# Performance work log

Measured on AMD Instinct MI355X. Metric: run time of the kernel, lower is better.

## Reference

```python
import jax, jax.numpy as jnp
import numpy as np

N_NODES = 50000
N_EDGES = 800000
IN_F = 128
HID = 32
HEADS = 8
N_CLASSES = 40
OUT_HEADS = 1
NEG_SLOPE = 0.2


def _glorot(key, shape):
    fan_in, fan_out = shape[0], int(np.prod(shape[1:]))
    s = jnp.sqrt(6.0 / (fan_in + fan_out))
    return jax.random.uniform(key, shape, jnp.float32, -s, s)


def setup_inputs() -> dict:
    key = jax.random.key(0)
    ks = jax.random.split(key, 12)
    x = jax.random.normal(ks[0], (N_NODES, IN_F), jnp.float32)
    src = jax.random.randint(ks[1], (N_EDGES,), 0, N_NODES, jnp.int32)
    dst = jax.random.randint(ks[2], (N_EDGES,), 0, N_NODES, jnp.int32)
    # layer 1: IN_F -> HEADS*HID
    W1 = _glorot(ks[3], (IN_F, HEADS * HID))
    al1 = _glorot(ks[4], (HEADS, HID))
    ar1 = _glorot(ks[5], (HEADS, HID))
    # layer 2: HEADS*HID -> HEADS*HID
    W2 = _glorot(ks[6], (HEADS * HID, HEADS * HID))
    al2 = _glorot(ks[7], (HEADS, HID))
    ar2 = _glorot(ks[8], (HEADS, HID))
    # output layer: HEADS*HID -> OUT_HEADS*N_CLASSES (mean over heads)
    Wo = _glorot(ks[9], (HEADS * HID, OUT_HEADS * N_CLASSES))
    alo = _glorot(ks[10], (OUT_HEADS, N_CLASSES))
    aro = _glorot(ks[11], (OUT_HEADS, N_CLASSES))
    return dict(x=x, src=src, dst=dst, W1=W1, al1=al1, ar1=ar1,
                W2=W2, al2=al2, ar2=ar2, Wo=Wo, alo=alo, aro=aro)


def gat_conv(x, src, dst, W, al, ar, concat):
    """Standard GAT layer: per-head projection, edge attention, segment softmax, scatter-sum."""
    N = x.shape[0]
    H, F = al.shape
    h = (x @ W).reshape(N, H, F)                         # [N,H,F]
    el = jnp.einsum('nhf,hf->nh', h, al)                 # [N,H]
    er = jnp.einsum('nhf,hf->nh', h, ar)                 # [N,H]
    e = jax.nn.leaky_relu(el[src] + er[dst], NEG_SLOPE)  # [E,H]
    m = jax.ops.segment_max(e, dst, num_segments=N)      # [N,H] per-dst max
    ex = jnp.exp(e - m[dst])                             # [E,H]
    s = jax.ops.segment_sum(ex, dst, num_segments=N)     # [N,H]
    alpha = ex / (s[dst] + 1e-16)                        # [E,H] softmax over in-edges
    out = jax.ops.segment_sum(h[src] * alpha[:, :, None], dst, num_segments=N)  # [N,H,F]
    return out.reshape(N, H * F) if concat else out.mean(axis=1)


def reference(x, src, dst, W1, al1, ar1, W2, al2, ar2, Wo, alo, aro):
    h = jax.nn.elu(gat_conv(x, src, dst, W1, al1, ar1, concat=True))
    h = jax.nn.elu(gat_conv(h, src, dst, W2, al2, ar2, concat=True))
    out = gat_conv(h, src, dst, Wo, alo, aro, concat=False)  # [N, N_CLASSES]
    return jax.nn.log_softmax(out, axis=1)
```

## Files before the change

### kernel.cpp

```cpp
#include <hip/hip_runtime.h>
#include <hip/hip_bf16.h>

#define N_NODES 50000
#define N_EDGES 800000

typedef __bf16 bf16x8 __attribute__((ext_vector_type(8)));
typedef float f32x4 __attribute__((ext_vector_type(4)));
typedef float f32x2 __attribute__((ext_vector_type(2)));

__device__ __forceinline__ float loadF(const void* p, size_t i, bool isbf) {
    return isbf ? __bfloat162float(((const __hip_bfloat16*)p)[i]) : ((const float*)p)[i];
}
__device__ __forceinline__ float bfbits2f(unsigned short u) {
    return __uint_as_float(((unsigned)u) << 16);
}
__device__ __forceinline__ unsigned short f2bfbits(float f) {
    __hip_bfloat16 h = __float2bfloat16(f);
    return *(unsigned short*)&h;
}
__device__ __forceinline__ void acc8_fp8(float ex, uint2 r, float* acc) {
    f32x2 p0 = __builtin_amdgcn_cvt_pk_f32_fp8(r.x, false);
    f32x2 p1 = __builtin_amdgcn_cvt_pk_f32_fp8(r.x, true);
    f32x2 p2 = __builtin_amdgcn_cvt_pk_f32_fp8(r.y, false);
    f32x2 p3 = __builtin_amdgcn_cvt_pk_f32_fp8(r.y, true);
    acc[0] += ex * p0.x; acc[1] += ex * p0.y;
    acc[2] += ex * p1.x; acc[3] += ex * p1.y;
    acc[4] += ex * p2.x; acc[5] += ex * p2.y;
    acc[6] += ex * p3.x; acc[7] += ex * p3.y;
}

__global__ void cvt_hist_k(const void* __restrict__ x, const void* __restrict__ W1,
                           const void* __restrict__ W2, const void* __restrict__ Wo,
                           unsigned short* __restrict__ Xb, unsigned short* __restrict__ W1f,
                           unsigned short* __restrict__ W2f, unsigned short* __restrict__ Wof,
                           int* __restrict__ flag, const int* __restrict__ dst,
                           int* __restrict__ cursor, unsigned short* __restrict__ erank) {
    __shared__ int s_flag;
    int t = threadIdx.x;
    if (t < 64) {
        const unsigned short* xw = (const unsigned short*)x;
        int cnt = 0;
        for (int i = t; i < 512; i += 64) {
            unsigned e = (xw[2 * i] >> 7) & 0xFFu;
            if (e >= 117u && e <= 134u) cnt++;
        }
        for (int off = 32; off; off >>= 1) cnt += __shfl_down(cnt, off, 64);
        if (t == 0) s_flag = (cnt >= 256) ? 1 : 0;
    }
    __syncthreads();
    bool bf = (s_flag != 0);
    int i = blockIdx.x * blockDim.x + t;
    if (i == 0) *flag = s_flag ? 1 : 0;
    if (i < 800000) {
        if (!bf) {
            const float* f = (const float*)x + (size_t)i * 8;
            unsigned short r[8];
            for (int j = 0; j < 8; ++j) r[j] = f2bfbits(f[j]);
            *(uint4*)(Xb + (size_t)i * 8) = *(uint4*)r;
        }
        return;
    }
    int u = i - 800000;
    if (u >= 14336) {
        int e = u - 14336;
        if (e < N_EDGES) {
            int r = atomicAdd(&cursor[dst[e]], 1);
            erank[e] = (unsigned short)r;
        }
        return;
    }
    const void* W; unsigned short* dstp; int Nf, Npad, s, rem;
    if (u < 4096)        { W = W1; dstp = W1f; Nf = 256; Npad = 256; s = u / 1024; rem = u % 1024; }
    else if (u < 12288)  { u -= 4096;  W = W2; dstp = W2f; Nf = 256; Npad = 256; s = u / 1024; rem = u % 1024; }
    else                 { u -= 12288; W = Wo; dstp = Wof; Nf = 40;  Npad = 64;  s = u / 256;  rem = u % 256; }
    int n = rem >> 2, quad = rem & 3;
    unsigned short r[8];
    for (int j = 0; j < 8; ++j) {
        int k = s * 32 + quad * 8 + j;
        r[j] = (n < Nf) ? f2bfbits(loadF(W, (size_t)k * Nf + n, bf)) : (unsigned short)0;
    }
    int uo = (s * Npad + n) * 4 + quad;
    *(uint4*)(dstp + (size_t)uo * 8) = *(uint4*)r;
}

__global__ __launch_bounds__(256)
void scanall_k(const int* __restrict__ deg, int* __restrict__ rowptr, int N, int E) {
    __shared__ int s[256];
    __shared__ int ws[4];
    __shared__ int s_off;
    int t = threadIdx.x, b = blockIdx.x;
    int base = b * 256;
    int acc = 0;
    for (int i = t; i < base; i += 256) acc += deg[i];
    int wave = t >> 6, lane = t & 63;
    for (int off = 32; off; off >>= 1) acc += __shfl_down(acc, off, 64);
    if (lane == 0) ws[wave] = acc;
    __syncthreads();
    if (t == 0) s_off = ws[0] + ws[1] + ws[2] + ws[3];
    __syncthreads();
    int g = base + t;
    int v = (g < N) ? deg[g] : 0;
    s[t] = v; __syncthreads();
    for (int off = 1; off < 256; off <<= 1) {
        int x = (t >= off) ? s[t - off] : 0;
        __syncthreads();
        s[t] += x;
        __syncthreads();
    }
    if (g < N) rowptr[g] = s_off + s[t] - v;
    if (b == 0 && t == 0) rowptr[N] = E;
}

template <int K_, int AMODE, int WROWS, int WCOLS, int NTW>
__device__ __forceinline__
void gemm_attn_body(int bx, int t,
                    const unsigned short* __restrict__ A, const unsigned short* __restrict__ Wf,
                    void* __restrict__ Cout, const void* __restrict__ al,
                    const void* __restrict__ ar, const int* __restrict__ flag,
                    float* __restrict__ el, float* __restrict__ er, int M, int Nfull, int Npad) {
    constexpr int S = K_ / 32;
    constexpr int RB = WROWS * 32;
    int wave = t >> 6, lane = t & 63;
    int wrow = wave / WCOLS, wcol = wave % WCOLS;
    int m16 = lane & 15, quad = lane >> 4;
    int rbase = bx * RB + wrow * 32;
    int cbase = wcol * NTW * 16;

    int aoff[2];
    for (int mt = 0; mt < 2; ++mt) {
        int gr = rbase + mt * 16 + m16;
        int grc = (gr < M) ? gr : (M - 1);
        aoff[mt] = grc * K_ + quad * 8;
    }
    int boff[NTW];
    for (int nt = 0; nt < NTW; ++nt) {
        int gc = cbase + nt * 16 + m16;
        boff[nt] = (gc * 4 + quad) * 8;
    }
    int bstep = Npad * 32;

    f32x4 acc[2][NTW] = {};
    bf16x8 a0[2], a1[2], b0[NTW], b1[NTW];
#pragma unroll
    for (int mt = 0; mt < 2; ++mt) a0[mt] = *(const bf16x8*)(A + aoff[mt]);
#pragma unroll
    for (int nt = 0; nt < NTW; ++nt) b0[nt] = *(const bf16x8*)(Wf + boff[nt]);
#pragma unroll
    for (int s = 0; s < S; ++s) {
        if (s + 1 < S) {
#pragma unroll
            for (int mt = 0; mt < 2; ++mt)
                a1[mt] = *(const bf16x8*)(A + aoff[mt] + (s + 1) * 32);
#pragma unroll
            for (int nt = 0; nt < NTW; ++nt)
                b1[nt] = *(const bf16x8*)(Wf + boff[nt] + (size_t)(s + 1) * bstep);
        }
#pragma unroll
        for (int mt = 0; mt < 2; ++mt)
#pragma unroll
            for (int nt = 0; nt < NTW; ++nt)
                acc[mt][nt] = __builtin_amdgcn_mfma_f32_16x16x32_bf16(
                    b0[nt], a0[mt], acc[mt][nt], 0, 0, 0);
        if (s + 1 < S) {
#pragma unroll
            for (int mt = 0; mt < 2; ++mt) a0[mt] = a1[mt];
#pragma unroll
            for (int nt = 0; nt < NTW; ++nt) b0[nt] = b1[nt];
        }
    }

    if (AMODE == 0) {
        unsigned char* C8 = (unsigned char*)Cout;
#pragma unroll
        for (int mt = 0; mt < 2; ++mt) {
            int gr = rbase + mt * 16 + m16;
            if (gr < M) {
#pragma unroll
                for (int nt = 0; nt < NTW; ++nt) {
                    int u = __builtin_amdgcn_cvt_pk_fp8_f32(acc[mt][nt][0], acc[mt][nt][1], 0, false);
                    u = __builtin_amdgcn_cvt_pk_fp8_f32(acc[mt][nt][2], acc[mt][nt][3], u, true);
                    *(int*)(C8 + (size_t)gr * 256 + cbase + nt * 16 + quad * 4) = u;
                }
            }
        }
    } else {
        __hip_bfloat16* C = (__hip_bfloat16*)Cout;
#pragma unroll
        for (int mt = 0; mt < 2; ++mt) {
            int gr = rbase + mt * 16 + m16;
            if (gr < M) {
#pragma unroll
                for (int nt = 0; nt < NTW; ++nt) {
                    ushort4 o;
                    o.x = f2bfbits(acc[mt][nt][0]);
                    o.y = f2bfbits(acc[mt][nt][1]);
                    o.z = f2bfbits(acc[mt][nt][2]);
                    o.w = f2bfbits(acc[mt][nt][3]);
                    *(ushort4*)((unsigned short*)C + (size_t)gr * Npad + cbase + nt * 16 + quad * 4) = o;
                }
            }
        }
    }

    bool bf = (*flag != 0);
    if (AMODE == 0) {
#pragma unroll
        for (int h = 0; h < NTW / 2; ++h) {
            float alc2[2][4], arc2[2][4];
#pragma unroll
            for (int j = 0; j < 2; ++j)
#pragma unroll
                for (int r = 0; r < 4; ++r) {
                    int gc = cbase + (2 * h + j) * 16 + quad * 4 + r;
                    bool ok = gc < Nfull;
                    alc2[j][r] = ok ? loadF(al, gc, bf) : 0.f;
                    arc2[j][r] = ok ? loadF(ar, gc, bf) : 0.f;
                }
#pragma unroll
            for (int mt = 0; mt < 2; ++mt) {
                float pl = 0.f, pr = 0.f;
#pragma unroll
                for (int j = 0; j < 2; ++j)
#pragma unroll
                    for (int r = 0; r < 4; ++r) {
                        pl += acc[mt][2 * h + j][r] * alc2[j][r];
                        pr += acc[mt][2 * h + j][r] * arc2[j][r];
                    }
                pl += __shfl_xor(pl, 16, 64); pl += __shfl_xor(pl, 32, 64);
                pr += __shfl_xor(pr, 16, 64); pr += __shfl_xor(pr, 32, 64);
                int gr = rbase + mt * 16 + m16;
                if (quad == 0 && gr < M) {
                    int habs = wcol * (NTW / 2) + h;
                    el[gr * 8 + habs] = pl;
                    er[gr * 8 + habs] = pr;
                }
            }
        }
    } else {
        float pl[2] = {0.f, 0.f}, pr[2] = {0.f, 0.f};
#pragma unroll
        for (int nt = 0; nt < NTW; ++nt) {
            float alc4[4], arc4[4];
#pragma unroll
            for (int r = 0; r < 4; ++r) {
                int gc = cbase + nt * 16 + quad * 4 + r;
                bool ok = gc < Nfull;
                alc4[r] = ok ? loadF(al, gc, bf) : 0.f;
                arc4[r] = ok ? loadF(ar, gc, bf) : 0.f;
            }
#pragma unroll
            for (int mt = 0; mt < 2; ++mt)
#pragma unroll
                for (int r = 0; r < 4; ++r) {
                    pl[mt] += acc[mt][nt][r] * alc4[r];
                    pr[mt] += acc[mt][nt][r] * arc4[r];
                }
        }
#pragma unroll
        for (int mt = 0; mt < 2; ++mt) {
            float l = pl[mt], r = pr[mt];
            l += __shfl_xor(l, 16, 64); l += __shfl_xor(l, 32, 64);
            r += __shfl_xor(r, 16, 64); r += __shfl_xor(r, 32, 64);
            int gr = rbase + mt * 16 + m16;
            if (quad == 0 && gr < M) { el[gr] = l; er[gr] = r; }
        }
    }
}

template <int K_, int AMODE, int WROWS, int WCOLS, int NTW>
__global__ __launch_bounds__(256, 2)
void gemm_attn_k(const unsigned short* __restrict__ A, const unsigned short* __restrict__ Wf,
                 void* __restrict__ Cout, const void* __restrict__ al,
                 const void* __restrict__ ar, const int* __restrict__ flag,
                 float* __restrict__ el, float* __restrict__ er, int M, int Nfull, int Npad) {
    gemm_attn_body<K_, AMODE, WROWS, WCOLS, NTW>(blockIdx.x, threadIdx.x,
                                                 A, Wf, Cout, al, ar, flag, el, er, M, Nfull, Npad);
}

__global__ __launch_bounds__(256, 2)
void scatter_gemm1_k(const unsigned short* __restrict__ A, const void* __restrict__ xraw,
                     const unsigned short* __restrict__ Wf,
                     void* __restrict__ Cout, const void* __restrict__ al,
                     const void* __restrict__ ar, const int* __restrict__ flag,
                     float* __restrict__ el, float* __restrict__ er, int M,
                     const int* __restrict__ src, const int* __restrict__ dst,
                     const int* __restrict__ rowptr, const unsigned short* __restrict__ erank,
                     int* __restrict__ ecol, int E, int GB) {
    int b = blockIdx.x, t = threadIdx.x;
    if (b < GB) {
        const unsigned short* Aeff = (*flag != 0) ? (const unsigned short*)xraw : A;
        gemm_attn_body<128, 0, 2, 2, 8>(b, t, Aeff, Wf, Cout, al, ar, flag, el, er, M, 256, 256);
    } else {
        int e = (b - GB) * 256 + t;
        if (e < E) {
            int d = dst[e];
            ecol[rowptr[d] + (int)erank[e]] = src[e];
        }
    }
}

__global__ __launch_bounds__(256)
void aggr1_k(const int* __restrict__ rowptr, const int* __restrict__ ecol,
             const float* __restrict__ el, const float* __restrict__ er,
             const unsigned char* __restrict__ Hp8, __hip_bfloat16* __restrict__ out, int N) {
    int t = threadIdx.x;
    int hw = t >> 5, l = t & 31;
    int n = blockIdx.x * 8 + hw;
    if (n >= N) return;
    int beg = rowptr[n], deg = rowptr[n + 1] - beg;

    int hh = l >> 2;
    float er_hh = er[n * 8 + hh];
    float ss = 0.f;
    float acc[8] = {0.f, 0.f, 0.f, 0.f, 0.f, 0.f, 0.f, 0.f};

    int i = 0;
    for (; i + 4 <= deg; i += 4) {
        int s0 = ecol[beg + i], s1 = ecol[beg + i + 1];
        int s2 = ecol[beg + i + 2], s3 = ecol[beg + i + 3];
        uint2 r0 = *(const uint2*)(Hp8 + (size_t)s0 * 256 + l * 8);
        uint2 r1 = *(const uint2*)(Hp8 + (size_t)s1 * 256 + l * 8);
        uint2 r2 = *(const uint2*)(Hp8 + (size_t)s2 * 256 + l * 8);
        uint2 r3 = *(const uint2*)(Hp8 + (size_t)s3 * 256 + l * 8);
        float v0 = el[s0 * 8 + hh] + er_hh;
        float v1 = el[s1 * 8 + hh] + er_hh;
        float v2 = el[s2 * 8 + hh] + er_hh;
        float v3 = el[s3 * 8 + hh] + er_hh;
        v0 = (v0 >= 0.f) ? v0 : 0.2f * v0;
        v1 = (v1 >= 0.f) ? v1 : 0.2f * v1;
        v2 = (v2 >= 0.f) ? v2 : 0.2f * v2;
        v3 = (v3 >= 0.f) ? v3 : 0.2f * v3;
        float e0 = __expf(v0), e1 = __expf(v1), e2 = __expf(v2), e3 = __expf(v3);
        ss += (e0 + e1) + (e2 + e3);
        acc8_fp8(e0, r0, acc);
        acc8_fp8(e1, r1, acc);
        acc8_fp8(e2, r2, acc);
        acc8_fp8(e3, r3, acc);
    }
    for (; i < deg; ++i) {
        int s0 = ecol[beg + i];
        uint2 r0 = *(const uint2*)(Hp8 + (size_t)s0 * 256 + l * 8);
        float v0 = el[s0 * 8 + hh] + er_hh;
        v0 = (v0 >= 0.f) ? v0 : 0.2f * v0;
        float e0 = __expf(v0);
        ss += e0;
        acc8_fp8(e0, r0, acc);
    }

    float inv = 1.f / (ss + 1e-16f);
    unsigned short o[8];
    for (int j = 0; j < 8; ++j) {
        float vv = acc[j] * inv;
        vv = (vv > 0.f) ? vv : expm1f(vv);
        o[j] = f2bfbits(vv);
    }
    *(uint4*)((unsigned short*)out + (size_t)n * 256 + l * 8) = *(uint4*)o;
}

__global__ __launch_bounds__(64)
void aggr_out_k(const int* __restrict__ rowptr, const int* __restrict__ ecol,
                const float* __restrict__ elo, const float* __restrict__ ero,
                const unsigned short* __restrict__ Hp64, void* __restrict__ outp,
                const int* __restrict__ flag, int N) {
    int n = blockIdx.x, l = threadIdx.x;
    int g = l >> 3, f = l & 7;
    int beg = rowptr[n], deg = rowptr[n + 1] - beg;
    float ero_n = ero[n];
    float ss = 0.f;
    float acc[8] = {0.f, 0.f, 0.f, 0.f, 0.f, 0.f, 0.f, 0.f};
    for (int i = g; i < deg; i += 8) {
        int s = ecol[beg + i];
        float v = elo[s] + ero_n;
        v = (v >= 0.f) ? v : 0.2f * v;
        float ex = __expf(v);
        ss += ex;
        uint4 r = *(const uint4*)(Hp64 + (size_t)s * 64 + f * 8);
        unsigned short u[8];
        *(uint4*)u = r;
        for (int j = 0; j < 8; ++j) acc[j] += ex * bfbits2f(u[j]);
    }
    for (int off = 8; off <= 32; off <<= 1) {
        ss += __shfl_xor(ss, off, 64);
        for (int j = 0; j < 8; ++j) acc[j] += __shfl_xor(acc[j], off, 64);
    }
    float inv = 1.f / (ss + 1e-16f);
    float r8[8];
    float vmax = -1e30f;
    for (int j = 0; j < 8; ++j) {
        r8[j] = acc[j] * inv;
        if (f < 5) vmax = fmaxf(vmax, r8[j]);
    }
    for (int off = 1; off <= 4; off <<= 1) vmax = fmaxf(vmax, __shfl_xor(vmax, off, 64));
    float es = 0.f;
    if (f < 5)
        for (int j = 0; j < 8; ++j) es += __expf(r8[j] - vmax);
    for (int off = 1; off <= 4; off <<= 1) es += __shfl_xor(es, off, 64);
    float lse = vmax + logf(es);
    if (f < 5 && g == 0) {
        if (*flag) {
            unsigned short o[8];
            for (int j = 0; j < 8; ++j) o[j] = f2bfbits(r8[j] - lse);
            *(uint4*)((unsigned short*)outp + (size_t)n * 40 + f * 8) = *(uint4*)o;
        } else {
            float* fo = (float*)outp + (size_t)n * 40 + f * 8;
            for (int j = 0; j < 8; ++j) fo[j] = r8[j] - lse;
        }
    }
}

extern "C" void kernel_launch(void* const* d_in, const int* in_sizes, int n_in,
                              void* d_out, int out_size, void* d_ws, size_t ws_size,
                              hipStream_t stream) {
    const int N = N_NODES, E = N_EDGES;
    const void* x   = d_in[0];
    const int* src  = (const int*)d_in[1];
    const int* dst  = (const int*)d_in[2];
    const void* W1  = d_in[3];
    const void* al1 = d_in[4];
    const void* ar1 = d_in[5];
    const void* W2  = d_in[6];
    const void* al2 = d_in[7];
    const void* ar2 = d_in[8];
    const void* Wo  = d_in[9];
    const void* alo = d_in[10];
    const void* aro = d_in[11];

    char* w = (char*)d_ws;
    auto alloc = [&](size_t bytes) { void* p = (void*)w; w += (bytes + 255) & ~(size_t)255; return p; };
    int* flag      = (int*)alloc(4);
    int* rowptr    = (int*)alloc((size_t)(N + 1) * 4);
    int* cursor    = (int*)alloc((size_t)N * 4);
    float* elo     = (float*)alloc((size_t)N * 4);
    float* ero     = (float*)alloc((size_t)N * 4);
    int* ecol      = (int*)alloc((size_t)E * 4);
    unsigned short* erank = (unsigned short*)alloc((size_t)E * 2);
    float* el      = (float*)alloc((size_t)N * 8 * 4);
    float* er      = (float*)alloc((size_t)N * 8 * 4);
    unsigned short* W1f = (unsigned short*)alloc((size_t)128 * 256 * 2);
    unsigned short* W2f = (unsigned short*)alloc((size_t)256 * 256 * 2);
    unsigned short* Wof = (unsigned short*)alloc((size_t)256 * 64 * 2);
    unsigned char* Hp8 = (unsigned char*)alloc((size_t)N * 256);
    __hip_bfloat16* Hagg = (__hip_bfloat16*)alloc((size_t)N * 256 * 2);
    unsigned short* Xb = (unsigned short*)Hagg;
    unsigned short* Hp64 = (unsigned short*)Hp8;

    int NB = (N + 255) / 256;
    int GB = (N + 63) / 64;
    int OB = (N + 127) / 128;
    int AB = (N + 7) / 8;
    int SB = (E + 255) / 256;
    int CVT_THREADS = 800000 + 14336 + E;

    hipMemsetAsync(cursor, 0, (size_t)N * 4, stream);
    cvt_hist_k<<<(CVT_THREADS + 255) / 256, 256, 0, stream>>>(
        x, W1, W2, Wo, Xb, W1f, W2f, Wof, flag, dst, cursor, erank);
    scanall_k<<<NB, 256, 0, stream>>>(cursor, rowptr, N, E);
    scatter_gemm1_k<<<GB + SB, 256, 0, stream>>>(
        Xb, x, W1f, Hp8, al1, ar1, flag, el, er, N, src, dst, rowptr, erank, ecol, E, GB);
    aggr1_k<<<AB, 256, 0, stream>>>(rowptr, ecol, el, er, Hp8, Hagg, N);
    gemm_attn_k<256, 0, 2, 2, 8><<<GB, 256, 0, stream>>>(
        (const unsigned short*)Hagg, W2f, Hp8, al2, ar2, flag, el, er, N, 256, 256);
    aggr1_k<<<AB, 256, 0, stream>>>(rowptr, ecol, el, er, Hp8, Hagg, N);
    gemm_attn_k<256, 1, 4, 1, 4><<<OB, 256, 0, stream>>>(
        (const unsigned short*)Hagg, Wof, Hp64, alo, aro, flag, elo, ero, N, 40, 64);
    aggr_out_k<<<N, 64, 0, stream>>>(rowptr, ecol, elo, ero, Hp64, d_out, flag, N);
}
```

Before: 354.3 us.

## Fuse fp32-to-bf16 conversion of x into layer-1 GEMM and regroup launches

Removes the separate pass that converted x from fp32 to bf16 into a staging buffer. The layer-1 GEMM now loads fp32 A fragments directly and converts them in registers. The edge histogram moves into the same launch as the GEMM, and the CSR scatter becomes its own kernel after the scan. This saves one full read and write of x, but adds a kernel launch and makes the GEMM read twice as many A bytes.

Measured after the change: 358.1 us. Within noise of the previous version (+1.1%).

```diff
diff --git a/kernel.cpp b/kernel.cpp
--- a/kernel.cpp
+++ b/kernel.cpp
@@ -7,6 +7,7 @@
 typedef __bf16 bf16x8 __attribute__((ext_vector_type(8)));
 typedef float f32x4 __attribute__((ext_vector_type(4)));
 typedef float f32x2 __attribute__((ext_vector_type(2)));
+typedef unsigned short u16x8 __attribute__((ext_vector_type(8)));
 
 __device__ __forceinline__ float loadF(const void* p, size_t i, bool isbf) {
     return isbf ? __bfloat162float(((const __hip_bfloat16*)p)[i]) : ((const float*)p)[i];
@@ -29,12 +30,11 @@
     acc[6] += ex * p3.x; acc[7] += ex * p3.y;
 }
 
-__global__ void cvt_hist_k(const void* __restrict__ x, const void* __restrict__ W1,
-                           const void* __restrict__ W2, const void* __restrict__ Wo,
-                           unsigned short* __restrict__ Xb, unsigned short* __restrict__ W1f,
-                           unsigned short* __restrict__ W2f, unsigned short* __restrict__ Wof,
-                           int* __restrict__ flag, const int* __restrict__ dst,
-                           int* __restrict__ cursor, unsigned short* __restrict__ erank) {
+__global__ __launch_bounds__(256)
+void cvtw_k(const void* __restrict__ x, const void* __restrict__ W1,
+            const void* __restrict__ W2, const void* __restrict__ Wo,
+            unsigned short* __restrict__ W1f, unsigned short* __restrict__ W2f,
+            unsigned short* __restrict__ Wof, int* __restrict__ flag) {
     __shared__ int s_flag;
     int t = threadIdx.x;
     if (t < 64) {
@@ -49,26 +49,9 @@
     }
     __syncthreads();
     bool bf = (s_flag != 0);
-    int i = blockIdx.x * blockDim.x + t;
-    if (i == 0) *flag = s_flag ? 1 : 0;
-    if (i < 800000) {
-        if (!bf) {
-            const float* f = (const float*)x + (size_t)i * 8;
-            unsigned short r[8];
-            for (int j = 0; j < 8; ++j) r[j] = f2bfbits(f[j]);
-            *(uint4*)(Xb + (size_t)i * 8) = *(uint4*)r;
-        }
-        return;
-    }
-    int u = i - 800000;
-    if (u >= 14336) {
-        int e = u - 14336;
-        if (e < N_EDGES) {
-            int r = atomicAdd(&cursor[dst[e]], 1);
-            erank[e] = (unsigned short)r;
-        }
-        return;
-    }
+    int u = blockIdx.x * blockDim.x + t;
+    if (u == 0) *flag = bf ? 1 : 0;
+    if (u >= 14336) return;
     const void* W; unsigned short* dstp; int Nf, Npad, s, rem;
     if (u < 4096)        { W = W1; dstp = W1f; Nf = 256; Npad = 256; s = u / 1024; rem = u % 1024; }
     else if (u < 12288)  { u -= 4096;  W = W2; dstp = W2f; Nf = 256; Npad = 256; s = u / 1024; rem = u % 1024; }
@@ -111,10 +94,27 @@
     if (b == 0 && t == 0) rowptr[N] = E;
 }
 
-template <int K_, int AMODE, int WROWS, int WCOLS, int NTW>
+template <bool AF32>
+__device__ __forceinline__ bf16x8 load_a_frag(const void* A, size_t off) {
+    if constexpr (!AF32) {
+        return *(const bf16x8*)((const unsigned short*)A + off);
+    } else {
+        const float* p = (const float*)A + off;
+        f32x4 v0 = *(const f32x4*)p;
+        f32x4 v1 = *(const f32x4*)(p + 4);
+        u16x8 u;
+        u[0] = f2bfbits(v0[0]); u[1] = f2bfbits(v0[1]);
+        u[2] = f2bfbits(v0[2]); u[3] = f2bfbits(v0[3]);
+        u[4] = f2bfbits(v1[0]); u[5] = f2bfbits(v1[1]);
+        u[6] = f2bfbits(v1[2]); u[7] = f2bfbits(v1[3]);
+        return __builtin_bit_cast(bf16x8, u);
+    }
+}
+
+template <int K_, int AMODE, int WROWS, int WCOLS, int NTW, bool AF32>
 __device__ __forceinline__
 void gemm_attn_body(int bx, int t,
-                    const unsigned short* __restrict__ A, const unsigned short* __restrict__ Wf,
+                    const void* __restrict__ A, const unsigned short* __restrict__ Wf,
                     void* __restrict__ Cout, const void* __restrict__ al,
                     const void* __restrict__ ar, const int* __restrict__ flag,
                     float* __restrict__ el, float* __restrict__ er, int M, int Nfull, int Npad) {
@@ -142,7 +142,7 @@
     f32x4 acc[2][NTW] = {};
     bf16x8 a0[2], a1[2], b0[NTW], b1[NTW];
 #pragma unroll
-    for (int mt = 0; mt < 2; ++mt) a0[mt] = *(const bf16x8*)(A + aoff[mt]);
+    for (int mt = 0; mt < 2; ++mt) a0[mt] = load_a_frag<AF32>(A, aoff[mt]);
 #pragma unroll
     for (int nt = 0; nt < NTW; ++nt) b0[nt] = *(const bf16x8*)(Wf + boff[nt]);
 #pragma unroll
@@ -150,7 +150,7 @@
         if (s + 1 < S) {
 #pragma unroll
             for (int mt = 0; mt < 2; ++mt)
-                a1[mt] = *(const bf16x8*)(A + aoff[mt] + (s + 1) * 32);
+                a1[mt] = load_a_frag<AF32>(A, aoff[mt] + (s + 1) * 32);
 #pragma unroll
             for (int nt = 0; nt < NTW; ++nt)
                 b1[nt] = *(const bf16x8*)(Wf + boff[nt] + (size_t)(s + 1) * bstep);
@@ -273,29 +273,38 @@
                  void* __restrict__ Cout, const void* __restrict__ al,
                  const void* __restrict__ ar, const int* __restrict__ flag,
                  float* __restrict__ el, float* __restrict__ er, int M, int Nfull, int Npad) {
-    gemm_attn_body<K_, AMODE, WROWS, WCOLS, NTW>(blockIdx.x, threadIdx.x,
-                                                 A, Wf, Cout, al, ar, flag, el, er, M, Nfull, Npad);
+    gemm_attn_body<K_, AMODE, WROWS, WCOLS, NTW, false>(blockIdx.x, threadIdx.x,
+                                                        A, Wf, Cout, al, ar, flag, el, er, M, Nfull, Npad);
 }
 
 __global__ __launch_bounds__(256, 2)
-void scatter_gemm1_k(const unsigned short* __restrict__ A, const void* __restrict__ xraw,
-                     const unsigned short* __restrict__ Wf,
-                     void* __restrict__ Cout, const void* __restrict__ al,
-                     const void* __restrict__ ar, const int* __restrict__ flag,
-                     float* __restrict__ el, float* __restrict__ er, int M,
-                     const int* __restrict__ src, const int* __restrict__ dst,
-                     const int* __restrict__ rowptr, const unsigned short* __restrict__ erank,
-                     int* __restrict__ ecol, int E, int GB) {
+void gemm1_hist_k(const void* __restrict__ xraw, const unsigned short* __restrict__ Wf,
+                  void* __restrict__ Cout, const void* __restrict__ al,
+                  const void* __restrict__ ar, const int* __restrict__ flag,
+                  float* __restrict__ el, float* __restrict__ er, int M,
+                  const int* __restrict__ dst, int* __restrict__ cursor,
+                  unsigned short* __restrict__ erank, int E, int HB) {
     int b = blockIdx.x, t = threadIdx.x;
-    if (b < GB) {
-        const unsigned short* Aeff = (*flag != 0) ? (const unsigned short*)xraw : A;
-        gemm_attn_body<128, 0, 2, 2, 8>(b, t, Aeff, Wf, Cout, al, ar, flag, el, er, M, 256, 256);
+    if (b < HB) {
+        int e = b * 256 + t;
+        if (e < E) erank[e] = (unsigned short)atomicAdd(&cursor[dst[e]], 1);
     } else {
-        int e = (b - GB) * 256 + t;
-        if (e < E) {
-            int d = dst[e];
-            ecol[rowptr[d] + (int)erank[e]] = src[e];
-        }
+        int gb = b - HB;
+        if (*flag != 0)
+            gemm_attn_body<128, 0, 2, 2, 8, false>(gb, t, xraw, Wf, Cout, al, ar, flag, el, er, M, 256, 256);
+        else
+            gemm_attn_body<128, 0, 2, 2, 8, true>(gb, t, xraw, Wf, Cout, al, ar, flag, el, er, M, 256, 256);
+    }
+}
+
+__global__ __launch_bounds__(256)
+void scatter_k(const int* __restrict__ src, const int* __restrict__ dst,
+               const int* __restrict__ rowptr, const unsigned short* __restrict__ erank,
+               int* __restrict__ ecol, int E) {
+    int e = blockIdx.x * 256 + threadIdx.x;
+    if (e < E) {
+        int d = dst[e];
+        ecol[rowptr[d] + (int)erank[e]] = src[e];
     }
 }
 
@@ -441,22 +450,21 @@
     unsigned short* Wof = (unsigned short*)alloc((size_t)256 * 64 * 2);
     unsigned char* Hp8 = (unsigned char*)alloc((size_t)N * 256);
     __hip_bfloat16* Hagg = (__hip_bfloat16*)alloc((size_t)N * 256 * 2);
-    unsigned short* Xb = (unsigned short*)Hagg;
     unsigned short* Hp64 = (unsigned short*)Hp8;
 
     int NB = (N + 255) / 256;
     int GB = (N + 63) / 64;
     int OB = (N + 127) / 128;
     int AB = (N + 7) / 8;
-    int SB = (E + 255) / 256;
-    int CVT_THREADS = 800000 + 14336 + E;
+    int HB = (E + 255) / 256;
+    int WVT = (14336 + 255) / 256;
 
     hipMemsetAsync(cursor, 0, (size_t)N * 4, stream);
-    cvt_hist_k<<<(CVT_THREADS + 255) / 256, 256, 0, stream>>>(
-        x, W1, W2, Wo, Xb, W1f, W2f, Wof, flag, dst, cursor, erank);
+    cvtw_k<<<WVT, 256, 0, stream>>>(x, W1, W2, Wo, W1f, W2f, Wof, flag);
+    gemm1_hist_k<<<HB + GB, 256, 0, stream>>>(
+        x, W1f, Hp8, al1, ar1, flag, el, er, N, dst, cursor, erank, E, HB);
     scanall_k<<<NB, 256, 0, stream>>>(cursor, rowptr, N, E);
-    scatter_gemm1_k<<<GB + SB, 256, 0, stream>>>(
-        Xb, x, W1f, Hp8, al1, ar1, flag, el, er, N, src, dst, rowptr, erank, ecol, E, GB);
+    scatter_k<<<HB, 256, 0, stream>>>(src, dst, rowptr, erank, ecol, E);
     aggr1_k<<<AB, 256, 0, stream>>>(rowptr, ecol, el, er, Hp8, Hagg, N);
     gemm_attn_k<256, 0, 2, 2, 8><<<GB, 256, 0, stream>>>(
         (const unsigned short*)Hagg, W2f, Hp8, al2, ar2, flag, el, er, N, 256, 256);
```
